# Optimization experiments

Hardware: AMD Instinct MI355X
Metric: run time of the kernel (lower is better)

## Reference

```python
import jax, jax.numpy as jnp
import numpy as np

DIM_Q = 512
DIM_K = 512
DIM_V = 512
NUM_HEADS = 8
EPS = 1e-5


def _layer_norm(x, g, b):
    m = jnp.mean(x, axis=-1, keepdims=True)
    v = jnp.mean(jnp.square(x - m), axis=-1, keepdims=True)
    return (x - m) * jax.lax.rsqrt(v + EPS) * g + b


def setup_inputs() -> dict:
    key = jax.random.key(0)
    ks = jax.random.split(key, 12)
    B, Sq, Sk = 32, 512, 512
    s_q = 1.0 / np.sqrt(DIM_Q)
    s_v = 1.0 / np.sqrt(DIM_V)
    return {
        "Q": jax.random.normal(ks[0], (B, Sq, DIM_Q), jnp.float32),
        "K": jax.random.normal(ks[1], (B, Sk, DIM_K), jnp.float32),
        "Wq": jax.random.normal(ks[2], (DIM_Q, DIM_V), jnp.float32) * s_q,
        "bq": jnp.zeros((DIM_V,), jnp.float32),
        "Wk": jax.random.normal(ks[3], (DIM_K, DIM_V), jnp.float32) * s_q,
        "bk": jnp.zeros((DIM_V,), jnp.float32),
        "Wv": jax.random.normal(ks[4], (DIM_K, DIM_V), jnp.float32) * s_q,
        "bv": jnp.zeros((DIM_V,), jnp.float32),
        "Wo": jax.random.normal(ks[5], (DIM_V, DIM_V), jnp.float32) * s_v,
        "bo": jnp.zeros((DIM_V,), jnp.float32),
        "ln0_g": jnp.ones((DIM_V,), jnp.float32),
        "ln0_b": jnp.zeros((DIM_V,), jnp.float32),
        "ln1_g": jnp.ones((DIM_V,), jnp.float32),
        "ln1_b": jnp.zeros((DIM_V,), jnp.float32),
    }


def reference(Q, K, Wq, bq, Wk, bk, Wv, bv, Wo, bo, ln0_g, ln0_b, ln1_g, ln1_b):
    B, Sq, _ = Q.shape
    Sk = K.shape[1]
    H = NUM_HEADS
    dh = DIM_V // H
    q = Q @ Wq + bq  # [B, Sq, V]
    k = K @ Wk + bk  # [B, Sk, V]
    v = K @ Wv + bv  # [B, Sk, V]
    # split(dim_split, 2) + cat(dim 0) == standard head split
    qh = q.reshape(B, Sq, H, dh)
    kh = k.reshape(B, Sk, H, dh)
    vh = v.reshape(B, Sk, H, dh)
    # NOTE: original scales by sqrt(dim_V), not sqrt(head_dim)
    scores = jnp.einsum("bqhd,bkhd->bhqk", qh, kh) / np.sqrt(DIM_V)
    A = jax.nn.softmax(scores, axis=-1)  # [B, H, Sq, Sk]
    oh = qh + jnp.einsum("bhqk,bkhd->bqhd", A, vh)  # residual inside heads
    O = oh.reshape(B, Sq, DIM_V)  # cat heads back along feature dim
    O = _layer_norm(O, ln0_g, ln0_b)
    O = O + jax.nn.relu(O @ Wo + bo)
    O = _layer_norm(O, ln1_g, ln1_b)
    return O
```

## Files before the change

kernel.cpp:

```cpp
#include <hip/hip_runtime.h>

#define NB 32
#define SEQ 512
#define DIM 512
#define NH 8
#define DH 64
#define MTOT (NB*SEQ)

typedef __attribute__((ext_vector_type(8))) __bf16 bf16x8;
typedef __attribute__((ext_vector_type(8))) short s16x8;
typedef __attribute__((ext_vector_type(4))) float f32x4;
typedef __attribute__((ext_vector_type(16))) float f32x16;
typedef __attribute__((ext_vector_type(4))) unsigned u32x4;

__device__ __forceinline__ float bf2f(short u) {
    union { float f; unsigned u; } x; x.u = ((unsigned)(unsigned short)u) << 16; return x.f;
}
__device__ __forceinline__ short f2bf(float f) {
    union { float f; unsigned u; } x; x.f = f;
    unsigned r = x.u + 0x7FFFu + ((x.u >> 16) & 1u);
    return (short)(r >> 16);
}

#define MFMA16(a,b,c) __builtin_amdgcn_mfma_f32_16x16x32_bf16(a,b,c,0,0,0)
#define MFMA32(a,b,c) __builtin_amdgcn_mfma_f32_32x32x16_bf16(a,b,c,0,0,0)

__device__ __forceinline__ void gload_lds16(const void* g, void* l) {
    __builtin_amdgcn_global_load_lds(
        (const __attribute__((address_space(1))) unsigned int*)g,
        (__attribute__((address_space(3))) unsigned int*)l, 16, 0, 0);
}
__device__ __forceinline__ unsigned cvt_pk_bf16(float lo, float hi) {
    unsigned r;
    asm("v_cvt_pk_bf16_f32 %0, %1, %2" : "=v"(r) : "v"(lo), "v"(hi));
    return r;
}

__global__ __launch_bounds__(256) void k_wprep(
    const float* __restrict__ Wq, const float* __restrict__ Wk,
    const float* __restrict__ Wv, const float* __restrict__ Wo,
    short* __restrict__ Wt)
{
    __shared__ float t[64][65];
    const float* W = blockIdx.z==0?Wq: blockIdx.z==1?Wk: blockIdx.z==2?Wv:Wo;
    short* out = Wt + (size_t)blockIdx.z*DIM*DIM;
    int k0 = blockIdx.x*64, n0 = blockIdx.y*64;
    int c = threadIdx.x & 63, r4 = threadIdx.x >> 6;
    #pragma unroll
    for (int i=0;i<16;i++){ int r = i*4 + r4; t[r][c] = W[(size_t)(k0+r)*DIM + n0 + c]; }
    __syncthreads();
    #pragma unroll
    for (int i=0;i<16;i++){ int r = i*4 + r4; out[(size_t)(n0+r)*DIM + k0 + c] = f2bf(t[c][r]); }
}

__global__ __launch_bounds__(256) void k_projqkv(
    const float* __restrict__ Q, const float* __restrict__ K,
    const short* __restrict__ Wt,
    const float* __restrict__ bq, const float* __restrict__ bk, const float* __restrict__ bv,
    short* __restrict__ qb, short* __restrict__ kb, short* __restrict__ vT)
{
    __shared__ __align__(16) char pool[34816];
    short* lds = (short*)pool;
    char* As = pool;
    char* Bs = pool + 16384;
    const int tid = threadIdx.x;
    const int wave = tid >> 6, lane = tid & 63;
    const int z = blockIdx.z;
    const float* A   = (z==0) ? Q : K;
    const short* W   = Wt + z*(DIM*DIM);
    const float* bia = (z==0)?bq:(z==1)?bk:bv;
    const int m0 = blockIdx.x*128, n0 = blockIdx.y*128;

    const float* srcA[4];
    #pragma unroll
    for (int i=0;i<4;i++) {
        int P = i*256 + tid, r = P>>3, pc = P&7, lc = pc ^ (r&7);
        srcA[i] = A + (size_t)(m0+r)*DIM + lc*4;
    }
    const short* srcB[2];
    #pragma unroll
    for (int i=0;i<2;i++) {
        int P = i*256 + tid, r = P>>2, c = P&3;
        srcB[i] = W + (size_t)(n0+r)*DIM + c*8;
    }

#define PSTAGE(T) do { \
        const int k0_ = (T)*32; \
        gload_lds16(srcA[0] + k0_, As +         wave*1024); \
        gload_lds16(srcA[1] + k0_, As +  4096 + wave*1024); \
        gload_lds16(srcA[2] + k0_, As +  8192 + wave*1024); \
        gload_lds16(srcA[3] + k0_, As + 12288 + wave*1024); \
        gload_lds16(srcB[0] + k0_, Bs +         wave*1024); \
        gload_lds16(srcB[1] + k0_, Bs +  4096 + wave*1024); \
    } while(0)

    const int wr = (wave>>1)*64, wc = (wave&1)*64;
    const int fr = lane & 15, kg = lane >> 4;

    f32x4 acc[4][4];
    #pragma unroll
    for (int i=0;i<4;i++)
        #pragma unroll
        for (int j=0;j<4;j++) acc[i][j] = (f32x4){0.f,0.f,0.f,0.f};

    PSTAGE(0);

    for (int t=0; t<16; ++t) {
        __syncthreads();
        float4 alo[4], ahi[4];
        #pragma unroll
        for (int f=0; f<4; ++f) {
            int R = wr + f*16 + fr;
            const char* base = As + R*128;
            alo[f] = *(const float4*)(base + ((((kg<<1)  ) ^ (R&7))<<4));
            ahi[f] = *(const float4*)(base + ((((kg<<1)|1) ^ (R&7))<<4));
        }
        bf16x8 bfr[4];
        #pragma unroll
        for (int f=0; f<4; ++f)
            bfr[f] = *(const bf16x8*)(Bs + (wc + f*16 + fr)*64 + kg*16);
        __syncthreads();
        if (t < 15) PSTAGE(t+1);
        bf16x8 af[4];
        #pragma unroll
        for (int f=0; f<4; ++f) {
            u32x4 pk = { cvt_pk_bf16(alo[f].x, alo[f].y), cvt_pk_bf16(alo[f].z, alo[f].w),
                         cvt_pk_bf16(ahi[f].x, ahi[f].y), cvt_pk_bf16(ahi[f].z, ahi[f].w) };
            af[f] = __builtin_bit_cast(bf16x8, pk);
        }
        #pragma unroll
        for (int i=0;i<4;i++)
            #pragma unroll
            for (int j=0;j<4;j++) acc[i][j] = MFMA16(af[i], bfr[j], acc[i][j]);
    }
#undef PSTAGE
    __syncthreads();

    const int r0 = (lane>>4)*4;
    #pragma unroll
    for (int i=0;i<4;i++)
        #pragma unroll
        for (int j=0;j<4;j++) {
            int row = wr + i*16 + r0;
            int col = wc + j*16 + fr;
            float bb = bia[n0 + col];
            #pragma unroll
            for (int r=0;r<4;r++) lds[(row+r)*136 + col] = f2bf(acc[i][j][r] + bb);
        }
    __syncthreads();
    if (z < 2) {
        short* out = (z==0)? qb : kb;
        int row = tid>>1, ch = (tid&1)*64;
        #pragma unroll
        for (int j=0;j<8;j++) {
            int col = ch + j*8;
            s16x8 v = *(s16x8*)&lds[row*136 + col];
            *(s16x8*)&out[(size_t)(m0+row)*DIM + n0 + col] = v;
        }
    } else {
        int c = tid>>1, sh = (tid&1)*64;
        int b = m0 >> 9;
        int h = (n0 + c) >> 6, d = (n0 + c) & 63;
        size_t base = ((size_t)(b*NH + h)*DH + d)*SEQ + (m0 & 511) + sh;
        #pragma unroll
        for (int i8=0;i8<8;i8++) {
            s16x8 tv;
            #pragma unroll
            for (int j=0;j<8;j++) tv[j] = lds[(sh + i8*8 + j)*136 + c];
            *(s16x8*)&vT[base + i8*8] = tv;
        }
    }
}

__global__ __launch_bounds__(256, 2) void k_attn(
    const short* __restrict__ qb, const short* __restrict__ kb,
    const short* __restrict__ vT, short* __restrict__ Oh)
{
    __shared__ short pool[9216];
    __shared__ float invLds[4][2][32];
    char* poolB = (char*)pool;
    const int tid = threadIdx.x, wave = tid>>6, lane = tid&63;
    const int l31 = lane & 31, hi = lane >> 5;
    const int b = blockIdx.z, h = blockIdx.y;
    const int bh = b*NH + h;
    const int bx = blockIdx.x;
    const float SCALE = 0.0441941738241592f;

    bf16x8 qf[2][4];
    #pragma unroll
    for (int u=0; u<2; ++u)
        #pragma unroll
        for (int d=0; d<4; ++d)
            qf[u][d] = *(const bf16x8*)&qb[(size_t)(b*SEQ + bx*256 + u*128 + wave*32 + l31)*DIM + h*DH + d*16 + hi*8];

    const short* gK0 = kb + (size_t)(b*SEQ + l31)*DIM + h*DH + wave*16 + hi*8;
    const short* gV0 = vT + ((size_t)bh*DH + (wave>>1)*32 + l31)*SEQ + (wave&1)*16 + hi*8;

    f32x16 o[2][2];
    #pragma unroll
    for (int u=0;u<2;u++)
        #pragma unroll
        for (int q=0;q<2;q++)
            #pragma unroll
            for (int r=0;r<16;r++) o[u][q][r]=0.f;
    float lsum[2] = {0.f, 0.f};

    gload_lds16(gK0,            poolB + wave*1024);
    gload_lds16(gV0,            poolB + 8192 + wave*1024);

    for (int kt=0; kt<16; ++kt) {
        const int p = kt & 1;
        __syncthreads();
        if (kt < 15) {
            gload_lds16(gK0 + (size_t)(kt+1)*32*DIM, poolB + (p^1)*4096 + wave*1024);
            gload_lds16(gV0 + (kt+1)*32,             poolB + 8192 + (p^1)*4096 + wave*1024);
        }
        const char* Kb = poolB + p*4096 + lane*16;
        bf16x8 kf0 = *(const bf16x8*)(Kb);
        bf16x8 kf1 = *(const bf16x8*)(Kb + 1024);
        bf16x8 kf2 = *(const bf16x8*)(Kb + 2048);
        bf16x8 kf3 = *(const bf16x8*)(Kb + 3072);
        const char* Vb = poolB + 8192 + p*4096 + lane*16;
        bf16x8 v00 = *(const bf16x8*)(Vb);
        bf16x8 v01 = *(const bf16x8*)(Vb + 1024);
        bf16x8 v10 = *(const bf16x8*)(Vb + 2048);
        bf16x8 v11 = *(const bf16x8*)(Vb + 3072);
        #pragma unroll
        for (int u=0; u<2; ++u) {
            f32x16 s;
            #pragma unroll
            for (int r=0;r<16;r++) s[r]=0.f;
            s = MFMA32(kf0, qf[u][0], s);
            s = MFMA32(kf1, qf[u][1], s);
            s = MFMA32(kf2, qf[u][2], s);
            s = MFMA32(kf3, qf[u][3], s);
            float pe[16];
            #pragma unroll
            for (int r=0;r<16;r++) { pe[r] = __expf(s[r]*SCALE - 3.0f); lsum[u] += pe[r]; }
            unsigned pk0 = cvt_pk_bf16(pe[0],  pe[1]);
            unsigned pk1 = cvt_pk_bf16(pe[2],  pe[3]);
            unsigned pk2 = cvt_pk_bf16(pe[4],  pe[5]);
            unsigned pk3 = cvt_pk_bf16(pe[6],  pe[7]);
            unsigned pk4 = cvt_pk_bf16(pe[8],  pe[9]);
            unsigned pk5 = cvt_pk_bf16(pe[10], pe[11]);
            unsigned pk6 = cvt_pk_bf16(pe[12], pe[13]);
            unsigned pk7 = cvt_pk_bf16(pe[14], pe[15]);
            asm("v_permlane32_swap_b32 %0, %1" : "+v"(pk0), "+v"(pk2));
            asm("v_permlane32_swap_b32 %0, %1" : "+v"(pk1), "+v"(pk3));
            asm("v_permlane32_swap_b32 %0, %1" : "+v"(pk4), "+v"(pk6));
            asm("v_permlane32_swap_b32 %0, %1" : "+v"(pk5), "+v"(pk7));
            u32x4 f0w = {pk0, pk1, pk2, pk3};
            u32x4 f1w = {pk4, pk5, pk6, pk7};
            bf16x8 F0 = __builtin_bit_cast(bf16x8, f0w);
            bf16x8 F1 = __builtin_bit_cast(bf16x8, f1w);
            o[u][0] = MFMA32(F0, v00, o[u][0]);
            o[u][0] = MFMA32(F1, v01, o[u][0]);
            o[u][1] = MFMA32(F0, v10, o[u][1]);
            o[u][1] = MFMA32(F1, v11, o[u][1]);
        }
    }
    float linv[2];
    #pragma unroll
    for (int u=0;u<2;u++) { float v = lsum[u]; v += __shfl_xor(v, 32); linv[u] = 1.0f / v; }
    __syncthreads();
    if (lane < 32) { invLds[wave][0][l31] = linv[0]; invLds[wave][1][l31] = linv[1]; }
    short* O = pool + wave*2304;
    #pragma unroll
    for (int u=0; u<2; ++u) {
        #pragma unroll
        for (int r=0;r<16;r++) {
            int q = (r&3) + 8*(r>>2) + 4*hi;
            float iq = invLds[wave][u][q];
            O[q*72 + l31]      = f2bf(o[u][0][r] * iq);
            O[q*72 + 32 + l31] = f2bf(o[u][1][r] * iq);
        }
        int rr = lane>>1, c0 = (lane&1)*32;
        size_t baseO = ((size_t)bh*SEQ + bx*256 + u*128 + wave*32 + rr)*DH + c0;
        #pragma unroll
        for (int j=0;j<4;j++) {
            s16x8 v = *(s16x8*)&O[rr*72 + c0 + j*8];
            *(s16x8*)&Oh[baseO + j*8] = v;
        }
    }
}

__global__ __launch_bounds__(256) void k_ln0(
    const short* __restrict__ qb, const short* __restrict__ Oh,
    const float* __restrict__ g, const float* __restrict__ bt,
    short* __restrict__ x0)
{
    int wave = threadIdx.x>>6, lane = threadIdx.x&63;
    int row = blockIdx.x*4 + wave;
    int b = row >> 9, s = row & 511;
    int f0 = lane*8;
    s16x8 qv = *(const s16x8*)&qb[(size_t)row*DIM + f0];
    int h = f0 >> 6, d = f0 & 63;
    s16x8 ov = *(const s16x8*)&Oh[((size_t)(b*NH+h)*SEQ + s)*DH + d];
    float x[8];
    float sm=0.f, sq=0.f;
    #pragma unroll
    for (int j=0;j<8;j++) { x[j] = bf2f(qv[j]) + bf2f(ov[j]); sm += x[j]; sq += x[j]*x[j]; }
    #pragma unroll
    for (int off=1; off<64; off<<=1) { sm += __shfl_xor(sm,off); sq += __shfl_xor(sq,off); }
    float mean = sm*(1.0f/512.0f);
    float var  = sq*(1.0f/512.0f) - mean*mean;
    float inv  = rsqrtf(var + 1e-5f);
    float4 g0 = *(const float4*)&g[f0],  g1 = *(const float4*)&g[f0+4];
    float4 t0 = *(const float4*)&bt[f0], t1 = *(const float4*)&bt[f0+4];
    s16x8 outv;
    outv[0]=f2bf((x[0]-mean)*inv*g0.x + t0.x); outv[1]=f2bf((x[1]-mean)*inv*g0.y + t0.y);
    outv[2]=f2bf((x[2]-mean)*inv*g0.z + t0.z); outv[3]=f2bf((x[3]-mean)*inv*g0.w + t0.w);
    outv[4]=f2bf((x[4]-mean)*inv*g1.x + t1.x); outv[5]=f2bf((x[5]-mean)*inv*g1.y + t1.y);
    outv[6]=f2bf((x[6]-mean)*inv*g1.z + t1.z); outv[7]=f2bf((x[7]-mean)*inv*g1.w + t1.w);
    *(s16x8*)&x0[(size_t)row*DIM + f0] = outv;
}

__global__ __launch_bounds__(512) void k_gemmy_ln(
    const short* __restrict__ x0, const short* __restrict__ Wto,
    const float* __restrict__ bo,
    const float* __restrict__ g, const float* __restrict__ bt,
    float* __restrict__ out)
{
    __shared__ __align__(16) char pool[73728];
    const int tid = threadIdx.x;
    const int wave = tid >> 6, lane = tid & 63;
    const int fr = lane & 15, g4 = lane >> 4;

    int L = ((int)blockIdx.x & 7)*32 + ((int)blockIdx.x >> 3);
    const int m0 = L*64;

    size_t srcA = 0;
    if (wave < 4) {
        int r = tid>>2, c = tid&3;
        srcA = (size_t)(m0 + r)*DIM + ((c ^ ((r>>1)&3))<<3);
    }
    size_t srcB[4];
    #pragma unroll
    for (int i=0;i<4;i++) {
        int s = i*512 + tid, r = s>>2, c = s&3;
        srcB[i] = (size_t)r*DIM + ((c ^ ((r>>1)&3))<<3);
    }

    f32x4 acc[16];
    #pragma unroll
    for (int j=0;j<16;j++) acc[j] = (f32x4){0.f,0.f,0.f,0.f};

#define GSTAGE(T, BUF) do { \
        const short* As_ = x0  + (T)*32; \
        const short* Bs_ = Wto + (T)*32; \
        if (wave < 4) gload_lds16(As_ + srcA, pool + (BUF)*4096 + wave*1024); \
        char* dB_ = pool + 8192 + (BUF)*32768; \
        gload_lds16(Bs_ + srcB[0], dB_ +     0 + wave*1024); \
        gload_lds16(Bs_ + srcB[1], dB_ +  8192 + wave*1024); \
        gload_lds16(Bs_ + srcB[2], dB_ + 16384 + wave*1024); \
        gload_lds16(Bs_ + srcB[3], dB_ + 24576 + wave*1024); \
    } while(0)

    GSTAGE(0, 0);
    __syncthreads();

    int cur = 0;
    for (int t=0; t<16; ++t) {
        if (t < 15) GSTAGE(t+1, cur^1);
        const char* pA = pool + cur*4096;
        const char* pB = pool + 8192 + cur*32768;
        int R = (wave>>1)*16 + fr;
        bf16x8 af = *(const bf16x8*)(pA + R*64 + ((g4 ^ ((R>>1)&3))<<4));
        #pragma unroll
        for (int j=0;j<16;j++) {
            int Rb = (wave&1)*256 + j*16 + fr;
            bf16x8 bf = *(const bf16x8*)(pB + Rb*64 + ((g4 ^ ((Rb>>1)&3))<<4));
            acc[j] = MFMA16(af, bf, acc[j]);
        }
        __syncthreads();
        cur ^= 1;
    }
#undef GSTAGE

    short (*Lo)[520] = (short(*)[520])pool;
    {
        int wrow = (wave>>1)*16 + g4*4;
        int cbase = (wave&1)*256;
        #pragma unroll
        for (int j=0;j<16;j++) {
            int col = cbase + j*16 + fr;
            float bb = bo[col];
            #pragma unroll
            for (int r=0;r<4;r++) {
                float vv = acc[j][r] + bb;
                vv = vv > 0.f ? vv : 0.f;
                Lo[wrow + r][col] = f2bf(vv);
            }
        }
    }
    __syncthreads();

    int f0 = lane*8;
    float4 gg0 = *(const float4*)&g[f0],  gg1 = *(const float4*)&g[f0+4];
    float4 tt0 = *(const float4*)&bt[f0], tt1 = *(const float4*)&bt[f0+4];
    #pragma unroll
    for (int rr=0; rr<8; ++rr) {
        int row = wave*8 + rr;
        s16x8 rv = *(s16x8*)&Lo[row][f0];
        s16x8 xv = *(const s16x8*)&x0[(size_t)(m0+row)*DIM + f0];
        float x[8];
        float sm=0.f, sq=0.f;
        #pragma unroll
        for (int j=0;j<8;j++) { x[j] = bf2f(rv[j]) + bf2f(xv[j]); sm += x[j]; sq += x[j]*x[j]; }
        #pragma unroll
        for (int off=1; off<64; off<<=1) { sm += __shfl_xor(sm,off); sq += __shfl_xor(sq,off); }
        float mean = sm*(1.0f/512.0f);
        float var  = sq*(1.0f/512.0f) - mean*mean;
        float inv  = rsqrtf(var + 1e-5f);
        float4 o0, o1;
        o0.x=(x[0]-mean)*inv*gg0.x + tt0.x; o0.y=(x[1]-mean)*inv*gg0.y + tt0.y;
        o0.z=(x[2]-mean)*inv*gg0.z + tt0.z; o0.w=(x[3]-mean)*inv*gg0.w + tt0.w;
        o1.x=(x[4]-mean)*inv*gg1.x + tt1.x; o1.y=(x[5]-mean)*inv*gg1.y + tt1.y;
        o1.z=(x[6]-mean)*inv*gg1.z + tt1.z; o1.w=(x[7]-mean)*inv*gg1.w + tt1.w;
        *(float4*)&out[(size_t)(m0+row)*DIM + f0]     = o0;
        *(float4*)&out[(size_t)(m0+row)*DIM + f0 + 4] = o1;
    }
}

extern "C" void kernel_launch(void* const* d_in, const int* in_sizes, int n_in,
                              void* d_out, int out_size, void* d_ws, size_t ws_size,
                              hipStream_t stream)
{
    const float* Q  = (const float*)d_in[0];
    const float* K  = (const float*)d_in[1];
    const float* Wq = (const float*)d_in[2];
    const float* bq = (const float*)d_in[3];
    const float* Wk = (const float*)d_in[4];
    const float* bk = (const float*)d_in[5];
    const float* Wv = (const float*)d_in[6];
    const float* bv = (const float*)d_in[7];
    const float* Wo = (const float*)d_in[8];
    const float* bo = (const float*)d_in[9];
    const float* g0 = (const float*)d_in[10];
    const float* be0= (const float*)d_in[11];
    const float* g1 = (const float*)d_in[12];
    const float* be1= (const float*)d_in[13];
    float* out = (float*)d_out;

    char* ws = (char*)d_ws;
    size_t off = 0;
    short* Wt = (short*)(ws + off); off += (size_t)4*DIM*DIM*2;
    short* qb = (short*)(ws + off); off += (size_t)MTOT*DIM*2;
    short* kb = (short*)(ws + off); off += (size_t)MTOT*DIM*2;
    short* vT = (short*)(ws + off); off += (size_t)MTOT*DIM*2;
    short* Oh = (short*)(ws + off); off += (size_t)MTOT*DIM*2;
    short* x0 = vT;

    k_wprep   <<<dim3(8,8,4),   256, 0, stream>>>(Wq,Wk,Wv,Wo,Wt);
    k_projqkv <<<dim3(128,4,3), 256, 0, stream>>>(Q,K,Wt,bq,bk,bv,qb,kb,vT);
    k_attn    <<<dim3(2,NH,NB), 256, 0, stream>>>(qb,kb,vT,Oh);
    k_ln0     <<<dim3(MTOT/4),  256, 0, stream>>>(qb,Oh,g0,be0,x0);
    k_gemmy_ln<<<dim3(256),     512, 0, stream>>>(x0, Wt + (size_t)3*DIM*DIM, bo, g1, be1, out);
}
```

Baseline: 139.7 us.

## Double-buffer LDS in QKV projection GEMM and swizzle B tile reads

The QKV projection kernel now keeps two LDS stages and prefetches two k-steps ahead, using explicit vmcnt waits and raw barriers so global-to-LDS loads overlap with MFMA work instead of draining every iteration. The B tile layout gets an XOR swizzle on its 16-byte chunks to reduce LDS bank conflicts on fragment reads. LDS use per block grows, which may reduce occupancy, and the hand-written waitcnt counts must match the number of outstanding loads per stage.

```diff
diff --git a/kernel.cpp b/kernel.cpp
--- a/kernel.cpp
+++ b/kernel.cpp
@@ -59,10 +59,8 @@
     const float* __restrict__ bq, const float* __restrict__ bk, const float* __restrict__ bv,
     short* __restrict__ qb, short* __restrict__ kb, short* __restrict__ vT)
 {
-    __shared__ __align__(16) char pool[34816];
+    __shared__ __align__(16) char pool[49152];
     short* lds = (short*)pool;
-    char* As = pool;
-    char* Bs = pool + 16384;
     const int tid = threadIdx.x;
     const int wave = tid >> 6, lane = tid & 63;
     const int z = blockIdx.z;
@@ -81,17 +79,19 @@
     #pragma unroll
     for (int i=0;i<2;i++) {
         int P = i*256 + tid, r = P>>2, c = P&3;
-        srcB[i] = W + (size_t)(n0+r)*DIM + c*8;
-    }
-
-#define PSTAGE(T) do { \
+        srcB[i] = W + (size_t)(n0+r)*DIM + ((c ^ ((r>>1)&3))<<3);
+    }
+
+#define PSTAGE(T, BUF) do { \
         const int k0_ = (T)*32; \
-        gload_lds16(srcA[0] + k0_, As +         wave*1024); \
-        gload_lds16(srcA[1] + k0_, As +  4096 + wave*1024); \
-        gload_lds16(srcA[2] + k0_, As +  8192 + wave*1024); \
-        gload_lds16(srcA[3] + k0_, As + 12288 + wave*1024); \
-        gload_lds16(srcB[0] + k0_, Bs +         wave*1024); \
-        gload_lds16(srcB[1] + k0_, Bs +  4096 + wave*1024); \
+        char* dA_ = pool + (BUF)*16384; \
+        char* dB_ = pool + 32768 + (BUF)*8192; \
+        gload_lds16(srcA[0] + k0_, dA_ +         wave*1024); \
+        gload_lds16(srcA[1] + k0_, dA_ +  4096 + wave*1024); \
+        gload_lds16(srcA[2] + k0_, dA_ +  8192 + wave*1024); \
+        gload_lds16(srcA[3] + k0_, dA_ + 12288 + wave*1024); \
+        gload_lds16(srcB[0] + k0_, dB_ +         wave*1024); \
+        gload_lds16(srcB[1] + k0_, dB_ +  4096 + wave*1024); \
     } while(0)
 
     const int wr = (wave>>1)*64, wc = (wave&1)*64;
@@ -103,24 +103,35 @@
         #pragma unroll
         for (int j=0;j<4;j++) acc[i][j] = (f32x4){0.f,0.f,0.f,0.f};
 
-    PSTAGE(0);
+    PSTAGE(0, 0);
+    PSTAGE(1, 1);
 
     for (int t=0; t<16; ++t) {
-        __syncthreads();
+        const int cur = t & 1;
+        if (t < 15) asm volatile("s_waitcnt vmcnt(6)" ::: "memory");
+        else        asm volatile("s_waitcnt vmcnt(0)" ::: "memory");
+        asm volatile("s_barrier" ::: "memory");
+
+        const char* pA = pool + cur*16384;
+        const char* pB = pool + 32768 + cur*8192;
         float4 alo[4], ahi[4];
         #pragma unroll
         for (int f=0; f<4; ++f) {
             int R = wr + f*16 + fr;
-            const char* base = As + R*128;
+            const char* base = pA + R*128;
             alo[f] = *(const float4*)(base + ((((kg<<1)  ) ^ (R&7))<<4));
             ahi[f] = *(const float4*)(base + ((((kg<<1)|1) ^ (R&7))<<4));
         }
         bf16x8 bfr[4];
         #pragma unroll
-        for (int f=0; f<4; ++f)
-            bfr[f] = *(const bf16x8*)(Bs + (wc + f*16 + fr)*64 + kg*16);
-        __syncthreads();
-        if (t < 15) PSTAGE(t+1);
+        for (int f=0; f<4; ++f) {
+            int Rb = wc + f*16 + fr;
+            bfr[f] = *(const bf16x8*)(pB + Rb*64 + ((kg ^ ((Rb>>1)&3))<<4));
+        }
+        asm volatile("s_waitcnt lgkmcnt(0)" ::: "memory");
+        asm volatile("s_barrier" ::: "memory");
+        if (t < 14) PSTAGE(t+2, cur);
+
         bf16x8 af[4];
         #pragma unroll
         for (int f=0; f<4; ++f) {
```

New measurement: 135.1 us. 1.03x faster.

## Split QKV projection into Q and fused K/V kernels sharing the K tile

Applied to the files above, without the earlier changes.

The combined QKV projection kernel is split into a Q-only kernel and a K/V kernel that loads each K input tile once into shared memory and runs both the Wk and Wv MFMA products on it. This halves global reads and fp32-to-bf16 conversions of the K activations. The weight tile layout in shared memory also gets an XOR swizzle to cut bank conflicts on B-fragment reads. In exchange the K/V kernel holds twice the accumulators, which raises register pressure and may lower occupancy, and it adds one extra kernel launch.

```diff
diff --git a/kernel.cpp b/kernel.cpp
--- a/kernel.cpp
+++ b/kernel.cpp
@@ -53,45 +53,37 @@
     for (int i=0;i<16;i++){ int r = i*4 + r4; out[(size_t)(n0+r)*DIM + k0 + c] = f2bf(t[c][r]); }
 }
 
-__global__ __launch_bounds__(256) void k_projqkv(
-    const float* __restrict__ Q, const float* __restrict__ K,
-    const short* __restrict__ Wt,
-    const float* __restrict__ bq, const float* __restrict__ bk, const float* __restrict__ bv,
-    short* __restrict__ qb, short* __restrict__ kb, short* __restrict__ vT)
+__global__ __launch_bounds__(256) void k_projq(
+    const float* __restrict__ Q, const short* __restrict__ Wq,
+    const float* __restrict__ bq, short* __restrict__ qb)
 {
     __shared__ __align__(16) char pool[34816];
     short* lds = (short*)pool;
-    char* As = pool;
-    char* Bs = pool + 16384;
     const int tid = threadIdx.x;
     const int wave = tid >> 6, lane = tid & 63;
-    const int z = blockIdx.z;
-    const float* A   = (z==0) ? Q : K;
-    const short* W   = Wt + z*(DIM*DIM);
-    const float* bia = (z==0)?bq:(z==1)?bk:bv;
     const int m0 = blockIdx.x*128, n0 = blockIdx.y*128;
 
     const float* srcA[4];
     #pragma unroll
     for (int i=0;i<4;i++) {
         int P = i*256 + tid, r = P>>3, pc = P&7, lc = pc ^ (r&7);
-        srcA[i] = A + (size_t)(m0+r)*DIM + lc*4;
+        srcA[i] = Q + (size_t)(m0+r)*DIM + lc*4;
     }
     const short* srcB[2];
     #pragma unroll
     for (int i=0;i<2;i++) {
         int P = i*256 + tid, r = P>>2, c = P&3;
-        srcB[i] = W + (size_t)(n0+r)*DIM + c*8;
+        srcB[i] = Wq + (size_t)(n0+r)*DIM + ((c ^ ((r>>1)&3))<<3);
     }
 
 #define PSTAGE(T) do { \
         const int k0_ = (T)*32; \
-        gload_lds16(srcA[0] + k0_, As +         wave*1024); \
-        gload_lds16(srcA[1] + k0_, As +  4096 + wave*1024); \
-        gload_lds16(srcA[2] + k0_, As +  8192 + wave*1024); \
-        gload_lds16(srcA[3] + k0_, As + 12288 + wave*1024); \
-        gload_lds16(srcB[0] + k0_, Bs +         wave*1024); \
-        gload_lds16(srcB[1] + k0_, Bs +  4096 + wave*1024); \
+        gload_lds16(srcA[0] + k0_, pool +         wave*1024); \
+        gload_lds16(srcA[1] + k0_, pool +  4096 + wave*1024); \
+        gload_lds16(srcA[2] + k0_, pool +  8192 + wave*1024); \
+        gload_lds16(srcA[3] + k0_, pool + 12288 + wave*1024); \
+        gload_lds16(srcB[0] + k0_, pool + 16384 +        wave*1024); \
+        gload_lds16(srcB[1] + k0_, pool + 16384 + 4096 + wave*1024); \
     } while(0)
 
     const int wr = (wave>>1)*64, wc = (wave&1)*64;
@@ -111,14 +103,16 @@
         #pragma unroll
         for (int f=0; f<4; ++f) {
             int R = wr + f*16 + fr;
-            const char* base = As + R*128;
+            const char* base = pool + R*128;
             alo[f] = *(const float4*)(base + ((((kg<<1)  ) ^ (R&7))<<4));
             ahi[f] = *(const float4*)(base + ((((kg<<1)|1) ^ (R&7))<<4));
         }
         bf16x8 bfr[4];
         #pragma unroll
-        for (int f=0; f<4; ++f)
-            bfr[f] = *(const bf16x8*)(Bs + (wc + f*16 + fr)*64 + kg*16);
+        for (int f=0; f<4; ++f) {
+            int Rb = wc + f*16 + fr;
+            bfr[f] = *(const bf16x8*)(pool + 16384 + Rb*64 + ((kg ^ ((Rb>>1)&3))<<4));
+        }
         __syncthreads();
         if (t < 15) PSTAGE(t+1);
         bf16x8 af[4];
@@ -143,21 +137,144 @@
         for (int j=0;j<4;j++) {
             int row = wr + i*16 + r0;
             int col = wc + j*16 + fr;
-            float bb = bia[n0 + col];
+            float bb = bq[n0 + col];
             #pragma unroll
             for (int r=0;r<4;r++) lds[(row+r)*136 + col] = f2bf(acc[i][j][r] + bb);
         }
     __syncthreads();
-    if (z < 2) {
-        short* out = (z==0)? qb : kb;
+    {
         int row = tid>>1, ch = (tid&1)*64;
         #pragma unroll
         for (int j=0;j<8;j++) {
             int col = ch + j*8;
             s16x8 v = *(s16x8*)&lds[row*136 + col];
-            *(s16x8*)&out[(size_t)(m0+row)*DIM + n0 + col] = v;
-        }
-    } else {
+            *(s16x8*)&qb[(size_t)(m0+row)*DIM + n0 + col] = v;
+        }
+    }
+}
+
+__global__ __launch_bounds__(256) void k_projkv(
+    const float* __restrict__ K,
+    const short* __restrict__ Wk, const short* __restrict__ Wv,
+    const float* __restrict__ bk, const float* __restrict__ bv,
+    short* __restrict__ kb, short* __restrict__ vT)
+{
+    __shared__ __align__(16) char pool[34816];
+    short* lds = (short*)pool;
+    const int tid = threadIdx.x;
+    const int wave = tid >> 6, lane = tid & 63;
+    const int m0 = blockIdx.x*128, n0 = blockIdx.y*128;
+
+    const float* srcA[4];
+    #pragma unroll
+    for (int i=0;i<4;i++) {
+        int P = i*256 + tid, r = P>>3, pc = P&7, lc = pc ^ (r&7);
+        srcA[i] = K + (size_t)(m0+r)*DIM + lc*4;
+    }
+    const short *srcBk[2], *srcBv[2];
+    #pragma unroll
+    for (int i=0;i<2;i++) {
+        int P = i*256 + tid, r = P>>2, c = P&3;
+        size_t o = (size_t)(n0+r)*DIM + ((c ^ ((r>>1)&3))<<3);
+        srcBk[i] = Wk + o;
+        srcBv[i] = Wv + o;
+    }
+
+#define PSTAGE(T) do { \
+        const int k0_ = (T)*32; \
+        gload_lds16(srcA[0]  + k0_, pool +         wave*1024); \
+        gload_lds16(srcA[1]  + k0_, pool +  4096 + wave*1024); \
+        gload_lds16(srcA[2]  + k0_, pool +  8192 + wave*1024); \
+        gload_lds16(srcA[3]  + k0_, pool + 12288 + wave*1024); \
+        gload_lds16(srcBk[0] + k0_, pool + 16384 +        wave*1024); \
+        gload_lds16(srcBk[1] + k0_, pool + 16384 + 4096 + wave*1024); \
+        gload_lds16(srcBv[0] + k0_, pool + 24576 +        wave*1024); \
+        gload_lds16(srcBv[1] + k0_, pool + 24576 + 4096 + wave*1024); \
+    } while(0)
+
+    const int wr = (wave>>1)*64, wc = (wave&1)*64;
+    const int fr = lane & 15, kg = lane >> 4;
+
+    f32x4 ak[4][4], av[4][4];
+    #pragma unroll
+    for (int i=0;i<4;i++)
+        #pragma unroll
+        for (int j=0;j<4;j++) { ak[i][j] = (f32x4){0.f,0.f,0.f,0.f}; av[i][j] = (f32x4){0.f,0.f,0.f,0.f}; }
+
+    PSTAGE(0);
+
+    for (int t=0; t<16; ++t) {
+        __syncthreads();
+        float4 alo[4], ahi[4];
+        #pragma unroll
+        for (int f=0; f<4; ++f) {
+            int R = wr + f*16 + fr;
+            const char* base = pool + R*128;
+            alo[f] = *(const float4*)(base + ((((kg<<1)  ) ^ (R&7))<<4));
+            ahi[f] = *(const float4*)(base + ((((kg<<1)|1) ^ (R&7))<<4));
+        }
+        bf16x8 bkf[4], bvf[4];
+        #pragma unroll
+        for (int f=0; f<4; ++f) {
+            int Rb = wc + f*16 + fr;
+            int off = Rb*64 + ((kg ^ ((Rb>>1)&3))<<4);
+            bkf[f] = *(const bf16x8*)(pool + 16384 + off);
+            bvf[f] = *(const bf16x8*)(pool + 24576 + off);
+        }
+        __syncthreads();
+        if (t < 15) PSTAGE(t+1);
+        bf16x8 af[4];
+        #pragma unroll
+        for (int f=0; f<4; ++f) {
+            u32x4 pk = { cvt_pk_bf16(alo[f].x, alo[f].y), cvt_pk_bf16(alo[f].z, alo[f].w),
+                         cvt_pk_bf16(ahi[f].x, ahi[f].y), cvt_pk_bf16(ahi[f].z, ahi[f].w) };
+            af[f] = __builtin_bit_cast(bf16x8, pk);
+        }
+        #pragma unroll
+        for (int i=0;i<4;i++)
+            #pragma unroll
+            for (int j=0;j<4;j++) {
+                ak[i][j] = MFMA16(af[i], bkf[j], ak[i][j]);
+                av[i][j] = MFMA16(af[i], bvf[j], av[i][j]);
+            }
+    }
+#undef PSTAGE
+    __syncthreads();
+
+    const int r0 = (lane>>4)*4;
+    #pragma unroll
+    for (int i=0;i<4;i++)
+        #pragma unroll
+        for (int j=0;j<4;j++) {
+            int row = wr + i*16 + r0;
+            int col = wc + j*16 + fr;
+            float bb = bk[n0 + col];
+            #pragma unroll
+            for (int r=0;r<4;r++) lds[(row+r)*136 + col] = f2bf(ak[i][j][r] + bb);
+        }
+    __syncthreads();
+    {
+        int row = tid>>1, ch = (tid&1)*64;
+        #pragma unroll
+        for (int j=0;j<8;j++) {
+            int col = ch + j*8;
+            s16x8 v = *(s16x8*)&lds[row*136 + col];
+            *(s16x8*)&kb[(size_t)(m0+row)*DIM + n0 + col] = v;
+        }
+    }
+    __syncthreads();
+    #pragma unroll
+    for (int i=0;i<4;i++)
+        #pragma unroll
+        for (int j=0;j<4;j++) {
+            int row = wr + i*16 + r0;
+            int col = wc + j*16 + fr;
+            float bb = bv[n0 + col];
+            #pragma unroll
+            for (int r=0;r<4;r++) lds[(row+r)*136 + col] = f2bf(av[i][j][r] + bb);
+        }
+    __syncthreads();
+    {
         int c = tid>>1, sh = (tid&1)*64;
         int b = m0 >> 9;
         int h = (n0 + c) >> 6, d = (n0 + c) & 63;
@@ -452,7 +569,8 @@
     short* x0 = vT;
 
     k_wprep   <<<dim3(8,8,4),   256, 0, stream>>>(Wq,Wk,Wv,Wo,Wt);
-    k_projqkv <<<dim3(128,4,3), 256, 0, stream>>>(Q,K,Wt,bq,bk,bv,qb,kb,vT);
+    k_projq   <<<dim3(128,4),   256, 0, stream>>>(Q, Wt, bq, qb);
+    k_projkv  <<<dim3(128,4),   256, 0, stream>>>(K, Wt + (size_t)1*DIM*DIM, Wt + (size_t)2*DIM*DIM, bk, bv, kb, vT);
     k_attn    <<<dim3(2,NH,NB), 256, 0, stream>>>(qb,kb,vT,Oh);
     k_ln0     <<<dim3(MTOT/4),  256, 0, stream>>>(qb,Oh,g0,be0,x0);
     k_gemmy_ln<<<dim3(256),     512, 0, stream>>>(x0, Wt + (size_t)3*DIM*DIM, bo, g1, be1, out);
```

Result: no change. 142.4 us (+2.0%).
